# Kernel optimization log

Hardware: AMD Instinct MI355X
Metric: run time of the kernel (lower is better)

## Reference

```python
import jax, jax.numpy as jnp
import numpy as np

B, T, D = 8, 4096, 768
N_HEADS = 12
HEAD_DIM = D // N_HEADS
N_STATE = 64
ALPHA = 0.1


def setup_inputs() -> dict:
    key = jax.random.key(0)
    k1, k2, k3 = jax.random.split(key, 3)
    H = jax.random.normal(k1, (B, T, D), dtype=jnp.float32)
    prototypes = jax.random.normal(k2, (N_STATE, D), dtype=jnp.float32)
    W_tok = jax.random.normal(k3, (D, D), dtype=jnp.float32) * (1.0 / np.sqrt(D))
    s0 = jnp.zeros((1, N_STATE, D), dtype=jnp.float32)
    return {"H": H, "prototypes": prototypes, "W_tok": W_tok, "s0": s0}


def reference(H, prototypes, W_tok, s0):
    b, t, d = H.shape
    hd = HEAD_DIM
    a = ALPHA
    # q: [B, n_heads, T, head_dim]
    q = (H @ W_tok.T).reshape(b, t, N_HEADS, hd).transpose(0, 2, 1, 3)
    # k: [n_heads, n_state, head_dim]
    k = prototypes.reshape(N_STATE, N_HEADS, hd).transpose(1, 0, 2)
    # score: [B, n_heads, T, n_state]; routing_temp == 1.0
    score = jnp.einsum('bhtd,hmd->bhtm', q, k) / (hd ** 0.5)
    w = jax.nn.softmax(score, axis=-1)
    g = 1.0 - a * w
    # suffix-inclusive product over T: prod_{t'>=t} g[t']
    suffix_inc = jnp.flip(jnp.cumprod(jnp.flip(g, axis=2), axis=2), axis=2)
    suffix_exc = jnp.concatenate(
        [suffix_inc[:, :, 1:, :], jnp.ones_like(suffix_inc[:, :, :1, :])], axis=2)
    w_eff = a * w * suffix_exc  # [B, H, T, n_state]
    h_ph = H.reshape(b, t, N_HEADS, hd).transpose(0, 2, 1, 3)  # [B,H,T,hd]
    s0h = jnp.broadcast_to(s0, (b, N_STATE, d)).reshape(
        b, N_STATE, N_HEADS, hd).transpose(0, 2, 1, 3)  # [B,H,n_state,hd]
    residual = suffix_inc[:, :, 0, :][..., None]  # [B,H,n_state,1]
    s = s0h * residual + jnp.einsum('bhtm,bhtd->bhmd', w_eff, h_ph)
    return s.transpose(0, 2, 1, 3).reshape(b, N_STATE, d)
```

## Files before the change

kernel.cpp:

```cpp
#include <hip/hip_runtime.h>

#define B_ 8
#define T_ 4096
#define D_ 768
#define NH_ 12
#define M_ 64
#define ALPHA_ 0.1f

#define CCH 16
#define CHUNK_T 256

using half8 = __attribute__((ext_vector_type(8))) _Float16;
using short8 = __attribute__((ext_vector_type(8))) short;
using f32x4 = __attribute__((ext_vector_type(4))) float;

__device__ __forceinline__ unsigned int f2h2(float a, float b) {
    unsigned short ua = __builtin_bit_cast(unsigned short, (_Float16)a);
    unsigned short ub = __builtin_bit_cast(unsigned short, (_Float16)b);
    return (unsigned int)ua | ((unsigned int)ub << 16);
}
__device__ __forceinline__ float h2f(unsigned short u) {
    return (float)__builtin_bit_cast(_Float16, u);
}
__device__ __forceinline__ void gload_lds16(const void* g, void* l) {
    __builtin_amdgcn_global_load_lds(
        (const __attribute__((address_space(1))) unsigned int*)g,
        (__attribute__((address_space(3))) unsigned int*)l, 16, 0, 0);
}

__global__ __launch_bounds__(256) void kH16(const float* __restrict__ H,
                                            unsigned short* __restrict__ H16) {
    const int i = blockIdx.x * 256 + threadIdx.x;
#pragma unroll
    for (int j = 0; j < 4; ++j) {
        const int idx = i + j * 1572864;
        const float4 v = reinterpret_cast<const float4*>(H)[idx];
        uint2 pk = {f2h2(v.x, v.y), f2h2(v.z, v.w)};
        reinterpret_cast<uint2*>(H16)[idx] = pk;
    }
}

__global__ __launch_bounds__(256) void kP(const float* __restrict__ proto,
                                          const float* __restrict__ W,
                                          unsigned short* __restrict__ P16) {
    const int et = blockIdx.x;
    const int h  = blockIdx.y;
    const int tid = threadIdx.x;

    __shared__ __align__(16) float Ws[64 * 128];
    __shared__ __align__(16) float Ks[64 * 64];

#pragma unroll
    for (int j = 0; j < 8; ++j) {
        int f = tid + j * 256;
        int i = f >> 5, c4 = f & 31;
        const float4 v = *reinterpret_cast<const float4*>(
            W + (size_t)(h * 64 + i) * D_ + et * 128 + c4 * 4);
        *reinterpret_cast<float4*>(&Ws[i * 128 + c4 * 4]) = v;
    }
#pragma unroll
    for (int j = 0; j < 4; ++j) {
        int f = tid + j * 256;
        int m = f >> 4, i4 = f & 15;
        const float4 v = *reinterpret_cast<const float4*>(
            proto + (size_t)m * D_ + h * 64 + i4 * 4);
        Ks[(i4 * 4 + 0) * 64 + m] = v.x;
        Ks[(i4 * 4 + 1) * 64 + m] = v.y;
        Ks[(i4 * 4 + 2) * 64 + m] = v.z;
        Ks[(i4 * 4 + 3) * 64 + m] = v.w;
    }
    __syncthreads();

    const int m0 = (tid >> 5) * 8;
    const int e0 = (tid & 31) * 4;
    float acc[8][4];
#pragma unroll
    for (int i = 0; i < 8; ++i)
#pragma unroll
        for (int j = 0; j < 4; ++j) acc[i][j] = 0.f;

    for (int i = 0; i < 64; ++i) {
        const float4 bb = *reinterpret_cast<const float4*>(&Ws[i * 128 + e0]);
        const float4 a0 = *reinterpret_cast<const float4*>(&Ks[i * 64 + m0]);
        const float4 a1 = *reinterpret_cast<const float4*>(&Ks[i * 64 + m0 + 4]);
        const float a[8] = {a0.x, a0.y, a0.z, a0.w, a1.x, a1.y, a1.z, a1.w};
#pragma unroll
        for (int mi = 0; mi < 8; ++mi) {
            acc[mi][0] = fmaf(a[mi], bb.x, acc[mi][0]);
            acc[mi][1] = fmaf(a[mi], bb.y, acc[mi][1]);
            acc[mi][2] = fmaf(a[mi], bb.z, acc[mi][2]);
            acc[mi][3] = fmaf(a[mi], bb.w, acc[mi][3]);
        }
    }
#pragma unroll
    for (int mi = 0; mi < 8; ++mi) {
        size_t idx = (size_t)(h * 64 + m0 + mi) * D_ + et * 128 + e0;
        uint2 pk = {f2h2(acc[mi][0] * 0.125f, acc[mi][1] * 0.125f),
                    f2h2(acc[mi][2] * 0.125f, acc[mi][3] * 0.125f)};
        *reinterpret_cast<uint2*>(P16 + idx) = pk;
    }
}

#define LDS_BYTES 51712

__global__ __launch_bounds__(256, 3) void k1(const unsigned short* __restrict__ H16,
                                             const unsigned short* __restrict__ P16,
                                             float* __restrict__ chunkprod,
                                             float* __restrict__ partial) {
    const int p = blockIdx.x;
    const int b = p & 7;
    const int s = p >> 3;
    const int h = s % 12;
    const int c = s / 12;
    const int tid = threadIdx.x;
    const int wv  = tid >> 6;
    const int lane = tid & 63;
    const int l15 = lane & 15;
    const int q4  = lane >> 4;

    extern __shared__ __align__(16) unsigned char smem[];
    unsigned short* wT = (unsigned short*)(smem);
    unsigned short* Hh = (unsigned short*)(smem + 33792);
    float* segprod = (float*)(smem + 50688);

    const size_t Hrow = (size_t)(b * T_ + c * CHUNK_T);
    const unsigned short* gA = H16 + Hrow * D_;
    const unsigned short* gB = P16 + (size_t)h * 64 * D_;

    f32x4 acc[4][4] = {};

    for (int kt = 0; kt < 12; ++kt) {
        __syncthreads();
#pragma unroll
        for (int j = 0; j < 8; ++j) {
            int sl = j * 256 + tid;
            int r = sl >> 3, gp = sl & 7, g = gp ^ (r & 7);
            gload_lds16(gA + (size_t)r * D_ + kt * 64 + g * 8, smem + sl * 16);
        }
#pragma unroll
        for (int j = 0; j < 2; ++j) {
            int sl = j * 256 + tid;
            int r = sl >> 3, gp = sl & 7, g = gp ^ (r & 7);
            gload_lds16(gB + (size_t)r * D_ + kt * 64 + g * 8, smem + 32768 + sl * 16);
        }
        __syncthreads();
#pragma unroll
        for (int ks = 0; ks < 2; ++ks) {
            const int gp = ((ks * 4 + q4) ^ (l15 & 7)) * 16;
            half8 af[4], bf[4];
#pragma unroll
            for (int tt = 0; tt < 4; ++tt)
                af[tt] = *reinterpret_cast<const half8*>(
                    smem + (wv * 64 + tt * 16 + l15) * 128 + gp);
#pragma unroll
            for (int mt = 0; mt < 4; ++mt)
                bf[mt] = *reinterpret_cast<const half8*>(
                    smem + 32768 + (mt * 16 + l15) * 128 + gp);
#pragma unroll
            for (int tt = 0; tt < 4; ++tt)
#pragma unroll
                for (int mt = 0; mt < 4; ++mt)
                    acc[tt][mt] = __builtin_amdgcn_mfma_f32_16x16x32_f16(
                        af[tt], bf[mt], acc[tt][mt], 0, 0, 0);
        }
    }
    __syncthreads();

#pragma unroll
    for (int tt = 0; tt < 4; ++tt)
#pragma unroll
        for (int rg = 0; rg < 4; ++rg) {
            float mx = fmaxf(fmaxf(acc[tt][0][rg], acc[tt][1][rg]),
                             fmaxf(acc[tt][2][rg], acc[tt][3][rg]));
#pragma unroll
            for (int msk = 1; msk <= 8; msk <<= 1)
                mx = fmaxf(mx, __shfl_xor(mx, msk, 64));
            float e0 = __expf(acc[tt][0][rg] - mx);
            float e1 = __expf(acc[tt][1][rg] - mx);
            float e2 = __expf(acc[tt][2][rg] - mx);
            float e3 = __expf(acc[tt][3][rg] - mx);
            float sm = (e0 + e1) + (e2 + e3);
#pragma unroll
            for (int msk = 1; msk <= 8; msk <<= 1)
                sm += __shfl_xor(sm, msk, 64);
            float inv = 1.0f / sm;
            acc[tt][0][rg] = e0 * inv;
            acc[tt][1][rg] = e1 * inv;
            acc[tt][2][rg] = e2 * inv;
            acc[tt][3][rg] = e3 * inv;
        }
#pragma unroll
    for (int tt = 0; tt < 4; ++tt)
#pragma unroll
        for (int mt = 0; mt < 4; ++mt) {
            uint2 pk = {f2h2(acc[tt][mt][0], acc[tt][mt][1]),
                        f2h2(acc[tt][mt][2], acc[tt][mt][3])};
            *reinterpret_cast<uint2*>(
                wT + (mt * 16 + l15) * 264 + wv * 64 + tt * 16 + q4 * 4) = pk;
        }
    __syncthreads();

    {
        const int g = tid >> 6, m_s = tid & 63;
        unsigned short* rowp = wT + m_s * 264 + g * 64;
        float pband = 1.0f;
#pragma unroll
        for (int oct = 0; oct < 8; ++oct) {
            short8 v = *reinterpret_cast<const short8*>(rowp + oct * 8);
#pragma unroll
            for (int j = 0; j < 8; ++j)
                pband *= fmaf(-ALPHA_, h2f((unsigned short)v[j]), 1.0f);
        }
        segprod[m_s * 4 + g] = pband;
        __syncthreads();
        float R = 1.0f;
#pragma unroll
        for (int gg = 1; gg < 4; ++gg)
            if (g + gg < 4) R *= segprod[m_s * 4 + g + gg];
#pragma unroll
        for (int oct = 7; oct >= 0; --oct) {
            short8 v = *reinterpret_cast<const short8*>(rowp + oct * 8);
            short8 o;
#pragma unroll
            for (int j = 7; j >= 0; --j) {
                float w = h2f((unsigned short)v[j]);
                _Float16 we = (_Float16)(ALPHA_ * w * R);
                o[j] = (short)__builtin_bit_cast(unsigned short, we);
                R *= fmaf(-ALPHA_, w, 1.0f);
            }
            *reinterpret_cast<short8*>(rowp + oct * 8) = o;
        }
    }
    __syncthreads();

    f32x4 pacc[4] = {};
    for (int hf = 0; hf < 2; ++hf) {
        if (hf) __syncthreads();
        {
            const int dp = tid & 15, tg = tid >> 4;
            const unsigned short* src = H16 + (Hrow + tg * 16) * D_
                                        + h * 64 + hf * 32 + 2 * dp;
            unsigned short* dst0 = Hh + (2 * dp) * 264 + tg * 16;
            unsigned short* dst1 = Hh + (2 * dp + 1) * 264 + tg * 16;
#pragma unroll
            for (int i = 0; i < 16; ++i) {
                unsigned int v = *reinterpret_cast<const unsigned int*>(src + (size_t)i * D_);
                dst0[i] = (unsigned short)(v & 0xffffu);
                dst1[i] = (unsigned short)(v >> 16);
            }
        }
        __syncthreads();
#pragma unroll
        for (int ks = 0; ks < 8; ++ks) {
            half8 a = *reinterpret_cast<const half8*>(
                wT + (wv * 16 + l15) * 264 + ks * 32 + q4 * 8);
#pragma unroll
            for (int dt = 0; dt < 2; ++dt) {
                half8 bb = *reinterpret_cast<const half8*>(
                    Hh + (dt * 16 + l15) * 264 + ks * 32 + q4 * 8);
                pacc[hf * 2 + dt] = __builtin_amdgcn_mfma_f32_16x16x32_f16(
                    a, bb, pacc[hf * 2 + dt], 0, 0, 0);
            }
        }
    }

    const int chunkIdx = (b * NH_ + h) * CCH + c;
    if (tid < 64)
        chunkprod[(size_t)chunkIdx * 64 + tid] =
            (segprod[tid * 4 + 0] * segprod[tid * 4 + 1]) *
            (segprod[tid * 4 + 2] * segprod[tid * 4 + 3]);
#pragma unroll
    for (int dt = 0; dt < 4; ++dt)
#pragma unroll
        for (int rg = 0; rg < 4; ++rg)
            partial[((size_t)chunkIdx * 64 + wv * 16 + q4 * 4 + rg) * 64 + dt * 16 + l15] =
                pacc[dt][rg];
}

__global__ __launch_bounds__(256) void k2(const float* __restrict__ chunkprod,
                                          const float* __restrict__ partial,
                                          const float* __restrict__ s0,
                                          float* __restrict__ out) {
    const int h = blockIdx.x;
    const int b = blockIdx.y;
    const int mg = blockIdx.z;
    const int tid = threadIdx.x;
    const int m  = mg * 16 + (tid >> 4);
    const int d0 = (tid & 15) * 4;

    const size_t cpBase = (size_t)(b * NH_ + h) * CCH;
    float sfx[CCH];
    float run = 1.0f;
#pragma unroll
    for (int c = CCH - 1; c >= 0; --c) {
        sfx[c] = run;
        run *= chunkprod[(cpBase + c) * M_ + m];
    }
    const float4 v0 = *reinterpret_cast<const float4*>(
        s0 + (size_t)m * D_ + h * 64 + d0);
    float4 acc = make_float4(v0.x * run, v0.y * run, v0.z * run, v0.w * run);
#pragma unroll
    for (int c = 0; c < CCH; ++c) {
        const float sv = sfx[c];
        const float4 pp = *reinterpret_cast<const float4*>(
            partial + ((cpBase + c) * M_ + m) * 64 + d0);
        acc.x = fmaf(sv, pp.x, acc.x);
        acc.y = fmaf(sv, pp.y, acc.y);
        acc.z = fmaf(sv, pp.z, acc.z);
        acc.w = fmaf(sv, pp.w, acc.w);
    }
    *reinterpret_cast<float4*>(out + (size_t)(b * M_ + m) * D_ + h * 64 + d0) = acc;
}

extern "C" void kernel_launch(void* const* d_in, const int* in_sizes, int n_in,
                              void* d_out, int out_size, void* d_ws, size_t ws_size,
                              hipStream_t stream) {
    const float* H     = (const float*)d_in[0];
    const float* proto = (const float*)d_in[1];
    const float* W     = (const float*)d_in[2];
    const float* s0    = (const float*)d_in[3];
    float* out = (float*)d_out;

    unsigned short* H16 = (unsigned short*)d_ws;
    unsigned short* P16 = (unsigned short*)((unsigned char*)d_ws + 50331648);
    float* chunkprod = (float*)((unsigned char*)d_ws + 51511296);
    float* partial   = (float*)((unsigned char*)d_ws + 51904512);

    kH16<<<dim3(6144), 256, 0, stream>>>(H, H16);
    kP<<<dim3(6, NH_), 256, 0, stream>>>(proto, W, P16);
    k1<<<dim3(1536), 256, LDS_BYTES, stream>>>(H16, P16, chunkprod, partial);
    k2<<<dim3(NH_, B_, 4), 256, 0, stream>>>(chunkprod, partial, s0, out);
}
```

Baseline: 232.5 us.

## Process two heads per block in k1 to share H tile loads

k1 now runs 512-thread blocks that each cover two heads for one (batch, chunk). The H tile is loaded once and reused by both heads' score GEMMs, which halves H global and LDS traffic and halves the block count. The scan and the w_eff·H GEMM are then done per head in sequence, with wider thread groups and paired 32-bit LDS stores for the H transpose. The softmax drops its max subtraction and uses a fast reciprocal. That removes shuffles but can overflow if scores are large, and it raises LDS use per block.

```diff
diff --git a/kernel.cpp b/kernel.cpp
--- a/kernel.cpp
+++ b/kernel.cpp
@@ -101,47 +101,50 @@
     }
 }
 
-#define LDS_BYTES 51712
-
-__global__ __launch_bounds__(256, 3) void k1(const unsigned short* __restrict__ H16,
+#define LDS_BYTES 69632
+
+__global__ __launch_bounds__(512, 4) void k1(const unsigned short* __restrict__ H16,
                                              const unsigned short* __restrict__ P16,
                                              float* __restrict__ chunkprod,
                                              float* __restrict__ partial) {
     const int p = blockIdx.x;
     const int b = p & 7;
     const int s = p >> 3;
-    const int h = s % 12;
-    const int c = s / 12;
+    const int hp = s % 6;
+    const int c  = s / 6;
     const int tid = threadIdx.x;
     const int wv  = tid >> 6;
     const int lane = tid & 63;
     const int l15 = lane & 15;
     const int q4  = lane >> 4;
+    const int hl  = wv >> 2;
+    const int tq  = wv & 3;
 
     extern __shared__ __align__(16) unsigned char smem[];
     unsigned short* wT = (unsigned short*)(smem);
     unsigned short* Hh = (unsigned short*)(smem + 33792);
-    float* segprod = (float*)(smem + 50688);
+    float* segprod = (float*)(smem + 67584);
 
     const size_t Hrow = (size_t)(b * T_ + c * CHUNK_T);
     const unsigned short* gA = H16 + Hrow * D_;
-    const unsigned short* gB = P16 + (size_t)h * 64 * D_;
+    const unsigned short* gB = P16 + (size_t)(hp * 2) * 64 * D_;
 
     f32x4 acc[4][4] = {};
 
     for (int kt = 0; kt < 12; ++kt) {
         __syncthreads();
 #pragma unroll
-        for (int j = 0; j < 8; ++j) {
-            int sl = j * 256 + tid;
+        for (int j = 0; j < 4; ++j) {
+            int sl = j * 512 + tid;
             int r = sl >> 3, gp = sl & 7, g = gp ^ (r & 7);
             gload_lds16(gA + (size_t)r * D_ + kt * 64 + g * 8, smem + sl * 16);
         }
 #pragma unroll
         for (int j = 0; j < 2; ++j) {
-            int sl = j * 256 + tid;
-            int r = sl >> 3, gp = sl & 7, g = gp ^ (r & 7);
-            gload_lds16(gB + (size_t)r * D_ + kt * 64 + g * 8, smem + 32768 + sl * 16);
+            int sl = j * 512 + tid;
+            int r = (sl & 511) >> 3, gp = sl & 7, g = gp ^ (r & 7);
+            gload_lds16(gB + (size_t)(j * 64 + r) * D_ + kt * 64 + g * 8,
+                        smem + 32768 + sl * 16);
         }
         __syncthreads();
 #pragma unroll
@@ -151,11 +154,11 @@
 #pragma unroll
             for (int tt = 0; tt < 4; ++tt)
                 af[tt] = *reinterpret_cast<const half8*>(
-                    smem + (wv * 64 + tt * 16 + l15) * 128 + gp);
+                    smem + (tq * 64 + tt * 16 + l15) * 128 + gp);
 #pragma unroll
             for (int mt = 0; mt < 4; ++mt)
                 bf[mt] = *reinterpret_cast<const half8*>(
-                    smem + 32768 + (mt * 16 + l15) * 128 + gp);
+                    smem + 32768 + hl * 8192 + (mt * 16 + l15) * 128 + gp);
 #pragma unroll
             for (int tt = 0; tt < 4; ++tt)
 #pragma unroll
@@ -164,117 +167,123 @@
                         af[tt], bf[mt], acc[tt][mt], 0, 0, 0);
         }
     }
-    __syncthreads();
 
 #pragma unroll
     for (int tt = 0; tt < 4; ++tt)
 #pragma unroll
         for (int rg = 0; rg < 4; ++rg) {
-            float mx = fmaxf(fmaxf(acc[tt][0][rg], acc[tt][1][rg]),
-                             fmaxf(acc[tt][2][rg], acc[tt][3][rg]));
-#pragma unroll
-            for (int msk = 1; msk <= 8; msk <<= 1)
-                mx = fmaxf(mx, __shfl_xor(mx, msk, 64));
-            float e0 = __expf(acc[tt][0][rg] - mx);
-            float e1 = __expf(acc[tt][1][rg] - mx);
-            float e2 = __expf(acc[tt][2][rg] - mx);
-            float e3 = __expf(acc[tt][3][rg] - mx);
+            float e0 = __expf(acc[tt][0][rg]);
+            float e1 = __expf(acc[tt][1][rg]);
+            float e2 = __expf(acc[tt][2][rg]);
+            float e3 = __expf(acc[tt][3][rg]);
             float sm = (e0 + e1) + (e2 + e3);
 #pragma unroll
             for (int msk = 1; msk <= 8; msk <<= 1)
                 sm += __shfl_xor(sm, msk, 64);
-            float inv = 1.0f / sm;
+            float inv = __builtin_amdgcn_rcpf(sm);
             acc[tt][0][rg] = e0 * inv;
             acc[tt][1][rg] = e1 * inv;
             acc[tt][2][rg] = e2 * inv;
             acc[tt][3][rg] = e3 * inv;
         }
-#pragma unroll
-    for (int tt = 0; tt < 4; ++tt)
-#pragma unroll
-        for (int mt = 0; mt < 4; ++mt) {
-            uint2 pk = {f2h2(acc[tt][mt][0], acc[tt][mt][1]),
-                        f2h2(acc[tt][mt][2], acc[tt][mt][3])};
-            *reinterpret_cast<uint2*>(
-                wT + (mt * 16 + l15) * 264 + wv * 64 + tt * 16 + q4 * 4) = pk;
-        }
     __syncthreads();
 
-    {
-        const int g = tid >> 6, m_s = tid & 63;
-        unsigned short* rowp = wT + m_s * 264 + g * 64;
-        float pband = 1.0f;
-#pragma unroll
-        for (int oct = 0; oct < 8; ++oct) {
-            short8 v = *reinterpret_cast<const short8*>(rowp + oct * 8);
-#pragma unroll
-            for (int j = 0; j < 8; ++j)
-                pband *= fmaf(-ALPHA_, h2f((unsigned short)v[j]), 1.0f);
-        }
-        segprod[m_s * 4 + g] = pband;
-        __syncthreads();
-        float R = 1.0f;
-#pragma unroll
-        for (int gg = 1; gg < 4; ++gg)
-            if (g + gg < 4) R *= segprod[m_s * 4 + g + gg];
-#pragma unroll
-        for (int oct = 7; oct >= 0; --oct) {
-            short8 v = *reinterpret_cast<const short8*>(rowp + oct * 8);
-            short8 o;
-#pragma unroll
-            for (int j = 7; j >= 0; --j) {
-                float w = h2f((unsigned short)v[j]);
-                _Float16 we = (_Float16)(ALPHA_ * w * R);
-                o[j] = (short)__builtin_bit_cast(unsigned short, we);
-                R *= fmaf(-ALPHA_, w, 1.0f);
-            }
-            *reinterpret_cast<short8*>(rowp + oct * 8) = o;
-        }
-    }
-    __syncthreads();
-
-    f32x4 pacc[4] = {};
-    for (int hf = 0; hf < 2; ++hf) {
-        if (hf) __syncthreads();
+    const int m_s = tid & 63;
+    const int g8  = tid >> 6;
+
+    for (int head = 0; head < 2; ++head) {
+        const int h = hp * 2 + head;
+        const int chunkIdx = (b * NH_ + h) * CCH + c;
+        if (head) __syncthreads();
+
+        if (hl == head) {
+#pragma unroll
+            for (int tt = 0; tt < 4; ++tt)
+#pragma unroll
+                for (int mt = 0; mt < 4; ++mt) {
+                    uint2 pk = {f2h2(acc[tt][mt][0], acc[tt][mt][1]),
+                                f2h2(acc[tt][mt][2], acc[tt][mt][3])};
+                    *reinterpret_cast<uint2*>(
+                        wT + (mt * 16 + l15) * 264 + tq * 64 + tt * 16 + q4 * 4) = pk;
+                }
+        }
         {
-            const int dp = tid & 15, tg = tid >> 4;
-            const unsigned short* src = H16 + (Hrow + tg * 16) * D_
-                                        + h * 64 + hf * 32 + 2 * dp;
+            const int dp = tid & 31, tg = tid >> 5;
+            const unsigned short* src = H16 + (Hrow + tg * 16) * D_ + h * 64 + 2 * dp;
             unsigned short* dst0 = Hh + (2 * dp) * 264 + tg * 16;
             unsigned short* dst1 = Hh + (2 * dp + 1) * 264 + tg * 16;
 #pragma unroll
-            for (int i = 0; i < 16; ++i) {
-                unsigned int v = *reinterpret_cast<const unsigned int*>(src + (size_t)i * D_);
-                dst0[i] = (unsigned short)(v & 0xffffu);
-                dst1[i] = (unsigned short)(v >> 16);
+            for (int i = 0; i < 8; ++i) {
+                unsigned int a = *reinterpret_cast<const unsigned int*>(
+                    src + (size_t)(2 * i) * D_);
+                unsigned int bb = *reinterpret_cast<const unsigned int*>(
+                    src + (size_t)(2 * i + 1) * D_);
+                *reinterpret_cast<unsigned int*>(dst0 + 2 * i) =
+                    (a & 0xffffu) | (bb << 16);
+                *reinterpret_cast<unsigned int*>(dst1 + 2 * i) =
+                    (a >> 16) | (bb & 0xffff0000u);
             }
         }
         __syncthreads();
-#pragma unroll
-        for (int ks = 0; ks < 8; ++ks) {
-            half8 a = *reinterpret_cast<const half8*>(
-                wT + (wv * 16 + l15) * 264 + ks * 32 + q4 * 8);
-#pragma unroll
-            for (int dt = 0; dt < 2; ++dt) {
-                half8 bb = *reinterpret_cast<const half8*>(
-                    Hh + (dt * 16 + l15) * 264 + ks * 32 + q4 * 8);
-                pacc[hf * 2 + dt] = __builtin_amdgcn_mfma_f32_16x16x32_f16(
-                    a, bb, pacc[hf * 2 + dt], 0, 0, 0);
+
+        {
+            unsigned short* rowp = wT + m_s * 264 + g8 * 32;
+            float pband = 1.0f;
+#pragma unroll
+            for (int oct = 0; oct < 4; ++oct) {
+                short8 v = *reinterpret_cast<const short8*>(rowp + oct * 8);
+#pragma unroll
+                for (int j = 0; j < 8; ++j)
+                    pband *= fmaf(-ALPHA_, h2f((unsigned short)v[j]), 1.0f);
             }
-        }
-    }
-
-    const int chunkIdx = (b * NH_ + h) * CCH + c;
-    if (tid < 64)
-        chunkprod[(size_t)chunkIdx * 64 + tid] =
-            (segprod[tid * 4 + 0] * segprod[tid * 4 + 1]) *
-            (segprod[tid * 4 + 2] * segprod[tid * 4 + 3]);
-#pragma unroll
-    for (int dt = 0; dt < 4; ++dt)
-#pragma unroll
-        for (int rg = 0; rg < 4; ++rg)
-            partial[((size_t)chunkIdx * 64 + wv * 16 + q4 * 4 + rg) * 64 + dt * 16 + l15] =
-                pacc[dt][rg];
+            segprod[g8 * 64 + m_s] = pband;
+            __syncthreads();
+            float R = 1.0f;
+#pragma unroll
+            for (int gg = 1; gg < 8; ++gg)
+                if (g8 + gg < 8) R *= segprod[(g8 + gg) * 64 + m_s];
+            if (g8 == 0)
+                chunkprod[(size_t)chunkIdx * 64 + m_s] = R * pband;
+#pragma unroll
+            for (int oct = 3; oct >= 0; --oct) {
+                short8 v = *reinterpret_cast<const short8*>(rowp + oct * 8);
+                short8 o;
+#pragma unroll
+                for (int j = 7; j >= 0; --j) {
+                    float w = h2f((unsigned short)v[j]);
+                    _Float16 we = (_Float16)(ALPHA_ * w * R);
+                    o[j] = (short)__builtin_bit_cast(unsigned short, we);
+                    R *= fmaf(-ALPHA_, w, 1.0f);
+                }
+                *reinterpret_cast<short8*>(rowp + oct * 8) = o;
+            }
+        }
+        __syncthreads();
+
+        {
+            const int mt = wv & 3;
+            const int dh = wv >> 2;
+            f32x4 pacc[2] = {};
+#pragma unroll
+            for (int ks = 0; ks < 8; ++ks) {
+                half8 a = *reinterpret_cast<const half8*>(
+                    wT + (mt * 16 + l15) * 264 + ks * 32 + q4 * 8);
+#pragma unroll
+                for (int dt = 0; dt < 2; ++dt) {
+                    half8 bb = *reinterpret_cast<const half8*>(
+                        Hh + (dh * 32 + dt * 16 + l15) * 264 + ks * 32 + q4 * 8);
+                    pacc[dt] = __builtin_amdgcn_mfma_f32_16x16x32_f16(
+                        a, bb, pacc[dt], 0, 0, 0);
+                }
+            }
+#pragma unroll
+            for (int dt = 0; dt < 2; ++dt)
+#pragma unroll
+                for (int rg = 0; rg < 4; ++rg)
+                    partial[((size_t)chunkIdx * 64 + mt * 16 + q4 * 4 + rg) * 64
+                            + dh * 32 + dt * 16 + l15] = pacc[dt][rg];
+        }
+    }
 }
 
 __global__ __launch_bounds__(256) void k2(const float* __restrict__ chunkprod,
@@ -328,6 +337,6 @@
 
     kH16<<<dim3(6144), 256, 0, stream>>>(H, H16);
     kP<<<dim3(6, NH_), 256, 0, stream>>>(proto, W, P16);
-    k1<<<dim3(1536), 256, LDS_BYTES, stream>>>(H16, P16, chunkprod, partial);
+    k1<<<dim3(768), 512, LDS_BYTES, stream>>>(H16, P16, chunkprod, partial);
     k2<<<dim3(NH_, B_, 4), 256, 0, stream>>>(chunkprod, partial, s0, out);
 }
```

Result: faster. 226.7 us (-2.5%).
